# Kernel optimization log

Hardware: AMD Instinct MI355X
Metric: run time of the kernel (lower is better)

The kernel has to match this reference:

```python
import jax, jax.numpy as jnp
import numpy as np
from jax import lax

B, T, D_IN, H, L, D_OUT = 64, 512, 256, 1024, 3, 128


def setup_inputs() -> dict:
    key = jax.random.key(0)
    ks = jax.random.split(key, 8)
    s_in = 1.0 / np.sqrt(H)  # PyTorch-style uniform-ish scale, keeps ReLU recurrence stable
    return {
        "x": jax.random.normal(ks[0], (B, T, D_IN), jnp.float32),
        "w_ih0": jax.random.normal(ks[1], (H, D_IN), jnp.float32) * s_in,
        "w_ih_rest": jax.random.normal(ks[2], (L - 1, H, H), jnp.float32) * s_in,
        "w_hh": jax.random.normal(ks[3], (L, H, H), jnp.float32) * s_in,
        "b_ih": jax.random.normal(ks[4], (L, H), jnp.float32) * s_in,
        "b_hh": jax.random.normal(ks[5], (L, H), jnp.float32) * s_in,
        "fc_w": jax.random.normal(ks[6], (D_OUT, H), jnp.float32) * s_in,
        "fc_b": jax.random.normal(ks[7], (D_OUT,), jnp.float32) * s_in,
    }


def _rnn_layer(seq, w_ih, w_hh, bi, bh):
    # seq: [B, T, d_in]; precompute input projection as one big GEMM
    pre = jnp.einsum("btd,hd->bth", seq, w_ih) + bi + bh  # [B, T, H]
    h0 = jnp.zeros((seq.shape[0], w_hh.shape[0]), seq.dtype)

    def step(h, p_t):  # h: [B, H], p_t: [B, H]
        h = jax.nn.relu(p_t + h @ w_hh.T)
        return h, h

    _, hs = lax.scan(step, h0, jnp.swapaxes(pre, 0, 1))  # [T, B, H]
    return jnp.swapaxes(hs, 0, 1)  # [B, T, H]


def reference(x, w_ih0, w_ih_rest, w_hh, b_ih, b_hh, fc_w, fc_b):
    seq = _rnn_layer(x, w_ih0, w_hh[0], b_ih[0], b_hh[0])
    for l in range(1, L):
        seq = _rnn_layer(seq, w_ih_rest[l - 1], w_hh[l], b_ih[l], b_hh[l])
    # fc on last timestep: out[:, -1, :] @ fc_w.T + fc_b
    return seq[:, -1, :] @ fc_w.T + fc_b
```

## Files before the change

kernel.cpp:

```cpp
#include <hip/hip_runtime.h>

#define NB   64
#define NT   512
#define DIN  256
#define NH   1024
#define DOUT 128

#define HS_STR 1028
#define RD_STR 136

typedef float f4 __attribute__((ext_vector_type(4)));
typedef float f2 __attribute__((ext_vector_type(2)));
typedef unsigned short bfr;

__device__ __forceinline__ float b2f(bfr u) {
    union { unsigned u; float f; } v; v.u = ((unsigned)u) << 16; return v.f;
}
__device__ __forceinline__ bfr f2b(float f) {
    union { float f; unsigned u; } v; v.f = f;
    unsigned r = v.u + 0x7FFFu + ((v.u >> 16) & 1u);
    return (bfr)(r >> 16);
}

template <typename T> __device__ __forceinline__ f4 load4(const T* p);
template <> __device__ __forceinline__ f4 load4<float>(const float* p) { return *(const f4*)p; }
template <> __device__ __forceinline__ f4 load4<bfr>(const bfr* p) {
    ushort4 u = *(const ushort4*)p;
    f4 r; r[0] = b2f(u.x); r[1] = b2f(u.y); r[2] = b2f(u.z); r[3] = b2f(u.w); return r;
}
template <typename T> __device__ __forceinline__ void store1(T* p, float v);
template <> __device__ __forceinline__ void store1<float>(float* p, float v) { *p = v; }
template <> __device__ __forceinline__ void store1<bfr>(bfr* p, float v) { *p = f2b(v); }
template <typename T> __device__ __forceinline__ float load1(const T* p);
template <> __device__ __forceinline__ float load1<float>(const float* p) { return *p; }
template <> __device__ __forceinline__ float load1<bfr>(const bfr* p) { return b2f(*p); }

template <int K, int LOG2CT, typename TA, typename TO>
__global__ __launch_bounds__(256)
void proj_kernel(const TA* __restrict__ A, const float* __restrict__ W,
                 const float* __restrict__ bih, const float* __restrict__ bhh,
                 TO* __restrict__ out, int tOff)
{
    __shared__ float As[16][68];
    __shared__ float Ws[16][68];
    const int tid = threadIdx.x;
    const int CTM = (1 << LOG2CT) - 1;
    const int m0 = (blockIdx.x >> 4) << 6;
    const int n0 = (blockIdx.x & 15) << 6;
    const int tm = tid & 15, tn = tid >> 4;
    const int lr = tid >> 2, lc = tid & 3;

    const int rA = m0 + lr;
    const long mrowA = (long)(rA >> LOG2CT) * NT + tOff + (rA & CTM);

    float acc[4][4] = {};
    for (int k0 = 0; k0 < K; k0 += 16) {
        f4 av = load4<TA>(&A[mrowA * K + k0 + lc * 4]);
        f4 wv = *(const f4*)&W[(n0 + lr) * K + k0 + lc * 4];
        __syncthreads();
        #pragma unroll
        for (int j = 0; j < 4; ++j) {
            As[lc * 4 + j][lr] = av[j];
            Ws[lc * 4 + j][lr] = wv[j];
        }
        __syncthreads();
        #pragma unroll
        for (int k = 0; k < 16; ++k) {
            f4 a = *(const f4*)&As[k][tm * 4];
            f4 w = *(const f4*)&Ws[k][tn * 4];
            #pragma unroll
            for (int i = 0; i < 4; ++i)
                #pragma unroll
                for (int j = 0; j < 4; ++j)
                    acc[i][j] += a[i] * w[j];
        }
    }
    #pragma unroll
    for (int j = 0; j < 4; ++j) {
        const int n = n0 + tn * 4 + j;
        const float bias = bih[n] + bhh[n];
        #pragma unroll
        for (int i = 0; i < 4; ++i)
            store1<TO>(&out[(long)(m0 + tm * 4 + i) * NH + n], acc[i][j] + bias);
    }
}

template <typename TP, int L2CT>
__global__ __launch_bounds__(256)
void copyback_kernel(const TP* __restrict__ Q, TP* __restrict__ P, int tOff)
{
    const int r = blockIdx.x, tid = threadIdx.x;
    const int b = r >> L2CT, t = r & ((1 << L2CT) - 1);
    const TP* q = Q + (long)r * NH;
    TP* p = P + ((long)b * NT + tOff + t) * NH;
    #pragma unroll
    for (int j = 0; j < 4; ++j) p[tid + j * 256] = q[tid + j * 256];
}

template <typename TP>
__global__ __launch_bounds__(512)
void recur_kernel(const float* __restrict__ Whh, TP* __restrict__ P,
                  float* __restrict__ Hring, unsigned* __restrict__ sy)
{
    __shared__ float hsA[8 * HS_STR];
    __shared__ float hsB[8 * HS_STR];
    __shared__ float red[32 * RD_STR];

    const int tid  = threadIdx.x;
    const int wg   = blockIdx.x;
    const int nBase = (wg & 63) << 4;
    const int set   = wg >> 6;
    const int rank  = wg & 63;
    const int lane  = tid & 63;
    const int tk = tid >> 4;
    const int tn = (tid >> 1) & 7;
    const int tb = tid & 1;
    const int bl = tid >> 4;
    const int nl = tid & 15;

    float w0[32], w1[32];
    {
        const float* p0 = &Whh[(nBase + tn * 2 + 0) * NH + tk * 32];
        const float* p1 = &Whh[(nBase + tn * 2 + 1) * NH + tk * 32];
        #pragma unroll
        for (int i = 0; i < 8; ++i) {
            *(f4*)&w0[i * 4] = *(const f4*)&p0[i * 4];
            *(f4*)&w1[i * 4] = *(const f4*)&p1[i * 4];
        }
    }
    for (int i = tid; i < 8 * HS_STR; i += 512) { hsA[i] = 0.f; hsB[i] = 0.f; }
    __syncthreads();

    #pragma unroll 1
    for (int ts = 0; ts < NT; ++ts) {
        const unsigned tgt = (unsigned)(ts + 1);

        float preA = 0.f; TP* ppA = nullptr;
        if (tid < 128) {
            ppA = &P[((long)(set * 16 + bl) * NT + ts) * NH + nBase + nl];
            preA = load1<TP>(ppA);
        }
        {
            float acc[4][2] = {};
            #pragma unroll
            for (int kk = 0; kk < 8; ++kk) {
                f4 hv[4];
                #pragma unroll
                for (int i = 0; i < 4; ++i)
                    hv[i] = *(const f4*)&hsA[(tb * 4 + i) * HS_STR + tk * 32 + kk * 4];
                #pragma unroll
                for (int c = 0; c < 4; ++c)
                    #pragma unroll
                    for (int i = 0; i < 4; ++i) {
                        acc[i][0] += hv[i][c] * w0[kk * 4 + c];
                        acc[i][1] += hv[i][c] * w1[kk * 4 + c];
                    }
            }
            #pragma unroll
            for (int i = 0; i < 4; ++i) {
                red[tk * RD_STR + (tb * 4 + i) * 16 + tn * 2 + 0] = acc[i][0];
                red[tk * RD_STR + (tb * 4 + i) * 16 + tn * 2 + 1] = acc[i][1];
            }
        }
        __syncthreads();
        if (tid < 128) {
            float s = 0.f;
            #pragma unroll
            for (int q = 0; q < 32; ++q) s += red[q * RD_STR + tid];
            const float h = fmaxf(s + preA, 0.f);
            store1<TP>(ppA, h);
            __hip_atomic_store(&Hring[((long)(ts & 1) << 16) + ((set * 16 + bl) << 10) + nBase + nl],
                               h, __ATOMIC_RELAXED, __HIP_MEMORY_SCOPE_AGENT);
        }
        __syncthreads();
        if (tid == 0 && ts < NT - 1)
            __hip_atomic_store(&sy[(set * 2 + 0) * 64 + rank], tgt,
                               __ATOMIC_RELAXED, __HIP_MEMORY_SCOPE_AGENT);

        float preB = 0.f; TP* ppB = nullptr;
        if (tid < 128) {
            ppB = &P[((long)(set * 16 + 8 + bl) * NT + ts) * NH + nBase + nl];
            preB = load1<TP>(ppB);
        }
        {
            float acc[4][2] = {};
            #pragma unroll
            for (int kk = 0; kk < 8; ++kk) {
                f4 hv[4];
                #pragma unroll
                for (int i = 0; i < 4; ++i)
                    hv[i] = *(const f4*)&hsB[(tb * 4 + i) * HS_STR + tk * 32 + kk * 4];
                #pragma unroll
                for (int c = 0; c < 4; ++c)
                    #pragma unroll
                    for (int i = 0; i < 4; ++i) {
                        acc[i][0] += hv[i][c] * w0[kk * 4 + c];
                        acc[i][1] += hv[i][c] * w1[kk * 4 + c];
                    }
            }
            __syncthreads();
            #pragma unroll
            for (int i = 0; i < 4; ++i) {
                red[tk * RD_STR + (tb * 4 + i) * 16 + tn * 2 + 0] = acc[i][0];
                red[tk * RD_STR + (tb * 4 + i) * 16 + tn * 2 + 1] = acc[i][1];
            }
        }
        __syncthreads();
        if (tid < 128) {
            float s = 0.f;
            #pragma unroll
            for (int q = 0; q < 32; ++q) s += red[q * RD_STR + tid];
            const float h = fmaxf(s + preB, 0.f);
            store1<TP>(ppB, h);
            __hip_atomic_store(&Hring[((long)(ts & 1) << 16) + ((set * 16 + 8 + bl) << 10) + nBase + nl],
                               h, __ATOMIC_RELAXED, __HIP_MEMORY_SCOPE_AGENT);
        }
        if (ts == NT - 1) break;
        __syncthreads();
        if (tid == 0)
            __hip_atomic_store(&sy[(set * 2 + 1) * 64 + rank], tgt,
                               __ATOMIC_RELAXED, __HIP_MEMORY_SCOPE_AGENT);

        {
            const unsigned* fpA = &sy[(set * 2 + 0) * 64 + lane];
            const unsigned* fpB = &sy[(set * 2 + 1) * 64 + lane];
            for (;;) {
                unsigned a = __hip_atomic_load(fpA, __ATOMIC_RELAXED, __HIP_MEMORY_SCOPE_AGENT);
                unsigned b = __hip_atomic_load(fpB, __ATOMIC_RELAXED, __HIP_MEMORY_SCOPE_AGENT);
                if (__all((int)(a >= tgt && b >= tgt))) break;
                __builtin_amdgcn_s_sleep(1);
            }
        }

        {
            const float* hbA = Hring + ((long)(ts & 1) << 16) + ((long)(set * 16) << 10) + (tid << 1);
            const float* hbB = hbA + (8 << 10);
            f2 sA[8], sB[8];
            #pragma unroll
            for (int r = 0; r < 8; ++r)
                asm volatile("global_load_dwordx2 %0, %1, off sc0 sc1"
                             : "=v"(sA[r]) : "v"(hbA + (r << 10)) : "memory");
            #pragma unroll
            for (int r = 0; r < 8; ++r)
                asm volatile("global_load_dwordx2 %0, %1, off sc0 sc1"
                             : "=v"(sB[r]) : "v"(hbB + (r << 10)) : "memory");
            asm volatile("s_waitcnt vmcnt(0)" ::: "memory");
            #pragma unroll
            for (int r = 0; r < 8; ++r) {
                *(f2*)&hsA[r * HS_STR + (tid << 1)] = sA[r];
                *(f2*)&hsB[r * HS_STR + (tid << 1)] = sB[r];
            }
        }
        __syncthreads();
    }
}

template <typename TP>
__global__ __launch_bounds__(128)
void fc_kernel(const TP* __restrict__ seq, const float* __restrict__ fcw,
               const float* __restrict__ fcb, float* __restrict__ out)
{
    __shared__ float hrow[NH];
    const int b = blockIdx.x, tid = threadIdx.x;
    for (int i = tid * 4; i < NH; i += 128 * 4) {
        f4 v = load4<TP>(&seq[((long)b * NT + (NT - 1)) * NH + i]);
        *(f4*)&hrow[i] = v;
    }
    __syncthreads();
    float s = 0.f;
    const float* wr = &fcw[tid * NH];
    for (int k = 0; k < NH; k += 4) {
        f4 w = *(const f4*)&wr[k];
        s += w[0] * hrow[k] + w[1] * hrow[k + 1] + w[2] * hrow[k + 2] + w[3] * hrow[k + 3];
    }
    out[b * DOUT + tid] = s + fcb[tid];
}

template <typename TP>
static void coop_recur(const float* W, TP* P, float* Hring, unsigned* sy,
                       hipStream_t stream)
{
    hipMemsetAsync(sy, 0, 4096, stream);
    const float* Wp = W; TP* Pp = P; float* H = Hring; unsigned* s = sy;
    void* args[4] = { &Wp, &Pp, &H, &s };
    hipLaunchCooperativeKernel((const void*)recur_kernel<TP>, dim3(256), dim3(512),
                               args, 0, stream);
}

static void run_pathA(const float* x, const float* wih0, const float* wihr,
                      const float* whh, const float* bih, const float* bhh,
                      const float* fcw, const float* fcb, float* out,
                      unsigned* sy, float* Hring, float* P0, float* P1,
                      hipStream_t stream)
{
    const dim3 blk(256);
    proj_kernel<DIN, 9, float, float><<<8192, blk, 0, stream>>>(x, wih0, bih, bhh, P0, 0);
    coop_recur<float>(whh, P0, Hring, sy, stream);
    proj_kernel<NH, 9, float, float><<<8192, blk, 0, stream>>>(P0, wihr,
        bih + NH, bhh + NH, P1, 0);
    coop_recur<float>(whh + NH * NH, P1, Hring, sy, stream);
    proj_kernel<NH, 9, float, float><<<8192, blk, 0, stream>>>(P1, wihr + NH * NH,
        bih + 2 * NH, bhh + 2 * NH, P0, 0);
    coop_recur<float>(whh + 2 * (NH * NH), P0, Hring, sy, stream);
    fc_kernel<float><<<dim3(NB), dim3(128), 0, stream>>>(P0, fcw, fcb, out);
}

template <typename TP>
static void run_pathBC(const float* x, const float* wih0, const float* wihr,
                       const float* whh, const float* bih, const float* bhh,
                       const float* fcw, const float* fcb, float* out,
                       unsigned* sy, float* Hring, TP* P, TP* Q, hipStream_t stream)
{
    const dim3 blk(256);
    proj_kernel<DIN, 9, float, TP><<<8192, blk, 0, stream>>>(x, wih0, bih, bhh, P, 0);
    coop_recur<TP>(whh, P, Hring, sy, stream);
    for (int l = 1; l < 3; ++l) {
        const float* wih = wihr + (long)(l - 1) * NH * NH;
        for (int c = 0; c < NT / 32; ++c) {
            proj_kernel<NH, 5, TP, TP><<<512, blk, 0, stream>>>(P, wih, bih + l * NH,
                                                                bhh + l * NH, Q, c * 32);
            copyback_kernel<TP, 5><<<NB * 32, blk, 0, stream>>>(Q, P, c * 32);
        }
        coop_recur<TP>(whh + (long)l * NH * NH, P, Hring, sy, stream);
    }
    fc_kernel<TP><<<dim3(NB), dim3(128), 0, stream>>>(P, fcw, fcb, out);
}

extern "C" void kernel_launch(void* const* d_in, const int* in_sizes, int n_in,
                              void* d_out, int out_size, void* d_ws, size_t ws_size,
                              hipStream_t stream)
{
    (void)in_sizes; (void)n_in; (void)out_size;
    const float* x    = (const float*)d_in[0];
    const float* wih0 = (const float*)d_in[1];
    const float* wihr = (const float*)d_in[2];
    const float* whh  = (const float*)d_in[3];
    const float* bih  = (const float*)d_in[4];
    const float* bhh  = (const float*)d_in[5];
    const float* fcw  = (const float*)d_in[6];
    const float* fcb  = (const float*)d_in[7];
    float* out = (float*)d_out;

    char* ws = (char*)d_ws;
    unsigned* sy = (unsigned*)ws;
    float* Hring = (float*)(ws + 4096);
    char* base = ws + 4096 + 2ull * NB * NH * 4;

    const size_t pF32 = (size_t)NB * NT * NH * 4;
    const size_t qF32 = (size_t)NB * 32 * NH * 4;
    const size_t head = 4096 + 2ull * NB * NH * 4;
    const size_t needA = head + 2 * pF32;
    const size_t needB = head + pF32 + qF32;

    if (ws_size >= needA) {
        float* P0 = (float*)base;
        float* P1 = (float*)(base + pF32);
        run_pathA(x, wih0, wihr, whh, bih, bhh, fcw, fcb, out,
                  sy, Hring, P0, P1, stream);
    } else if (ws_size >= needB) {
        float* P = (float*)base;
        float* Q = (float*)(base + pF32);
        run_pathBC<float>(x, wih0, wihr, whh, bih, bhh, fcw, fcb, out,
                          sy, Hring, P, Q, stream);
    } else {
        bfr* P = (bfr*)base;
        bfr* Q = (bfr*)(base + pF32 / 2);
        run_pathBC<bfr>(x, wih0, wihr, whh, bih, bhh, fcw, fcb, out,
                        sy, Hring, P, Q, stream);
    }
}
```

Baseline: 12.30 ms.

## Pipeline batch halves in recurrence so each half's exchange overlaps the other's compute

Restructures the persistent recurrence loop so the two batch halves (A and B) are staggered. Each half publishes its own per-wave ready flags and fetches its hidden state separately, so the poll and global load for one half run while the other half's matvec is in flight. The single full barrier plus combined poll per timestep is removed. The hidden-state tile is also re-laid out in LDS with padding every 32 floats to cut bank conflicts, and flags are polled as 64-bit pairs. The cost is more subtle cross-workgroup ordering and a larger LDS footprint.

New measurement: 10.90 ms. 11.4% less time.

```diff
diff --git a/kernel.cpp b/kernel.cpp
--- a/kernel.cpp
+++ b/kernel.cpp
@@ -6,11 +6,10 @@
 #define NH   1024
 #define DOUT 128
 
-#define HS_STR 1028
-#define RD_STR 136
+#define HS2_STR 1156
+#define RD_STR  136
 
 typedef float f4 __attribute__((ext_vector_type(4)));
-typedef float f2 __attribute__((ext_vector_type(2)));
 typedef unsigned short bfr;
 
 __device__ __forceinline__ float b2f(bfr u) {
@@ -97,13 +96,25 @@
     for (int j = 0; j < 4; ++j) p[tid + j * 256] = q[tid + j * 256];
 }
 
+__device__ __forceinline__ void poll64(const unsigned* fl, unsigned tgt, int lane)
+{
+    const unsigned long long* fp = (const unsigned long long*)fl + lane;
+    for (;;) {
+        unsigned long long v = __hip_atomic_load(fp, __ATOMIC_RELAXED,
+                                                 __HIP_MEMORY_SCOPE_AGENT);
+        unsigned lo = (unsigned)v, hi = (unsigned)(v >> 32);
+        if (__all((int)(lo >= tgt && hi >= tgt))) break;
+        __builtin_amdgcn_s_sleep(1);
+    }
+}
+
 template <typename TP>
 __global__ __launch_bounds__(512)
 void recur_kernel(const float* __restrict__ Whh, TP* __restrict__ P,
                   float* __restrict__ Hring, unsigned* __restrict__ sy)
 {
-    __shared__ float hsA[8 * HS_STR];
-    __shared__ float hsB[8 * HS_STR];
+    __shared__ float hsA[8 * HS2_STR];
+    __shared__ float hsB[8 * HS2_STR];
     __shared__ float red[32 * RD_STR];
 
     const int tid  = threadIdx.x;
@@ -112,11 +123,16 @@
     const int set   = wg >> 6;
     const int rank  = wg & 63;
     const int lane  = tid & 63;
-    const int tk = tid >> 4;
-    const int tn = (tid >> 1) & 7;
-    const int tb = tid & 1;
-    const int bl = tid >> 4;
-    const int nl = tid & 15;
+    const int tk = tid >> 4, tn = (tid >> 1) & 7, tb = tid & 1;
+    const int bl = tid >> 4, nl = tid & 15;
+    const int srow = tid >> 6;
+    const int sgOff = srow * NH + lane * 4;
+    const int slOff = srow * HS2_STR + lane * 4 + ((lane >> 3) << 2);
+
+    unsigned* syA = sy + (set * 2 + 0) * 128;
+    unsigned* syB = sy + (set * 2 + 1) * 128;
+    float* HrA = Hring + (long)(set * 16) * NH;
+    float* HrB = HrA + 8 * NH;
 
     float w0[32], w1[32];
     {
@@ -128,129 +144,135 @@
             *(f4*)&w1[i * 4] = *(const f4*)&p1[i * 4];
         }
     }
-    for (int i = tid; i < 8 * HS_STR; i += 512) { hsA[i] = 0.f; hsB[i] = 0.f; }
+    for (int i = tid; i < 8 * HS2_STR; i += 512) { hsA[i] = 0.f; hsB[i] = 0.f; }
     __syncthreads();
 
     #pragma unroll 1
     for (int ts = 0; ts < NT; ++ts) {
-        const unsigned tgt = (unsigned)(ts + 1);
-
-        float preA = 0.f; TP* ppA = nullptr;
+        const int slot = (ts & 1) * (NB * NH);
+        const int pslot = ((ts - 1) & 1) * (NB * NH);
+
+        float preA = 0.f, preB = 0.f; TP *ppA = nullptr, *ppB = nullptr;
         if (tid < 128) {
             ppA = &P[((long)(set * 16 + bl) * NT + ts) * NH + nBase + nl];
+            ppB = &P[((long)(set * 16 + 8 + bl) * NT + ts) * NH + nBase + nl];
             preA = load1<TP>(ppA);
-        }
-        {
-            float acc[4][2] = {};
-            #pragma unroll
-            for (int kk = 0; kk < 8; ++kk) {
-                f4 hv[4];
+            preB = load1<TP>(ppB);
+        }
+
+        float accA[4][2] = {};
+        #pragma unroll
+        for (int kk = 0; kk < 8; ++kk) {
+            const int kko = tk * 36 + kk * 4;
+            f4 hv[4];
+            #pragma unroll
+            for (int i = 0; i < 4; ++i)
+                hv[i] = *(const f4*)&hsA[(tb * 4 + i) * HS2_STR + kko];
+            #pragma unroll
+            for (int c = 0; c < 4; ++c)
                 #pragma unroll
-                for (int i = 0; i < 4; ++i)
-                    hv[i] = *(const f4*)&hsA[(tb * 4 + i) * HS_STR + tk * 32 + kk * 4];
-                #pragma unroll
-                for (int c = 0; c < 4; ++c)
-                    #pragma unroll
-                    for (int i = 0; i < 4; ++i) {
-                        acc[i][0] += hv[i][c] * w0[kk * 4 + c];
-                        acc[i][1] += hv[i][c] * w1[kk * 4 + c];
-                    }
-            }
-            #pragma unroll
-            for (int i = 0; i < 4; ++i) {
-                red[tk * RD_STR + (tb * 4 + i) * 16 + tn * 2 + 0] = acc[i][0];
-                red[tk * RD_STR + (tb * 4 + i) * 16 + tn * 2 + 1] = acc[i][1];
-            }
-        }
-        __syncthreads();
+                for (int i = 0; i < 4; ++i) {
+                    accA[i][0] += hv[i][c] * w0[kk * 4 + c];
+                    accA[i][1] += hv[i][c] * w1[kk * 4 + c];
+                }
+        }
+
+        f4 sB[4];
+        if (ts > 0) {
+            poll64(syB, (unsigned)ts, lane);
+            const float* src = HrB + pslot + sgOff;
+            #pragma unroll
+            for (int q = 0; q < 4; ++q)
+                asm volatile("global_load_dwordx4 %0, %1, off sc0 sc1"
+                             : "=v"(sB[q]) : "v"(src + q * 256) : "memory");
+        }
+
+        #pragma unroll
+        for (int i = 0; i < 4; ++i) {
+            float* rp = &red[tk * RD_STR + (tb * 4 + i) * 16 + tn * 2];
+            rp[0] = accA[i][0]; rp[1] = accA[i][1];
+        }
+        __syncthreads();
+
         if (tid < 128) {
             float s = 0.f;
             #pragma unroll
             for (int q = 0; q < 32; ++q) s += red[q * RD_STR + tid];
             const float h = fmaxf(s + preA, 0.f);
             store1<TP>(ppA, h);
-            __hip_atomic_store(&Hring[((long)(ts & 1) << 16) + ((set * 16 + bl) << 10) + nBase + nl],
-                               h, __ATOMIC_RELAXED, __HIP_MEMORY_SCOPE_AGENT);
-        }
-        __syncthreads();
-        if (tid == 0 && ts < NT - 1)
-            __hip_atomic_store(&sy[(set * 2 + 0) * 64 + rank], tgt,
+            __hip_atomic_store(&HrA[slot + bl * NH + nBase + nl], h,
                                __ATOMIC_RELAXED, __HIP_MEMORY_SCOPE_AGENT);
-
-        float preB = 0.f; TP* ppB = nullptr;
-        if (tid < 128) {
-            ppB = &P[((long)(set * 16 + 8 + bl) * NT + ts) * NH + nBase + nl];
-            preB = load1<TP>(ppB);
-        }
-        {
-            float acc[4][2] = {};
-            #pragma unroll
-            for (int kk = 0; kk < 8; ++kk) {
-                f4 hv[4];
+            if (ts < NT - 1) {
+                asm volatile("s_waitcnt vmcnt(0)" ::: "memory");
+                if (lane == 0)
+                    __hip_atomic_store(&syA[rank * 2 + (tid >> 6)], (unsigned)(ts + 1),
+                                       __ATOMIC_RELAXED, __HIP_MEMORY_SCOPE_AGENT);
+            }
+        }
+
+        if (ts > 0) {
+            asm volatile("s_waitcnt vmcnt(0)" ::: "memory");
+            #pragma unroll
+            for (int q = 0; q < 4; ++q)
+                *(f4*)&hsB[slOff + q * 288] = sB[q];
+        }
+        __syncthreads();
+
+        float accB[4][2] = {};
+        #pragma unroll
+        for (int kk = 0; kk < 8; ++kk) {
+            const int kko = tk * 36 + kk * 4;
+            f4 hv[4];
+            #pragma unroll
+            for (int i = 0; i < 4; ++i)
+                hv[i] = *(const f4*)&hsB[(tb * 4 + i) * HS2_STR + kko];
+            #pragma unroll
+            for (int c = 0; c < 4; ++c)
                 #pragma unroll
-                for (int i = 0; i < 4; ++i)
-                    hv[i] = *(const f4*)&hsB[(tb * 4 + i) * HS_STR + tk * 32 + kk * 4];
-                #pragma unroll
-                for (int c = 0; c < 4; ++c)
-                    #pragma unroll
-                    for (int i = 0; i < 4; ++i) {
-                        acc[i][0] += hv[i][c] * w0[kk * 4 + c];
-                        acc[i][1] += hv[i][c] * w1[kk * 4 + c];
-                    }
-            }
-            __syncthreads();
-            #pragma unroll
-            for (int i = 0; i < 4; ++i) {
-                red[tk * RD_STR + (tb * 4 + i) * 16 + tn * 2 + 0] = acc[i][0];
-                red[tk * RD_STR + (tb * 4 + i) * 16 + tn * 2 + 1] = acc[i][1];
-            }
-        }
-        __syncthreads();
+                for (int i = 0; i < 4; ++i) {
+                    accB[i][0] += hv[i][c] * w0[kk * 4 + c];
+                    accB[i][1] += hv[i][c] * w1[kk * 4 + c];
+                }
+        }
+
+        f4 sA[4];
+        if (ts < NT - 1) {
+            poll64(syA, (unsigned)(ts + 1), lane);
+            const float* src = HrA + slot + sgOff;
+            #pragma unroll
+            for (int q = 0; q < 4; ++q)
+                asm volatile("global_load_dwordx4 %0, %1, off sc0 sc1"
+                             : "=v"(sA[q]) : "v"(src + q * 256) : "memory");
+        }
+
+        #pragma unroll
+        for (int i = 0; i < 4; ++i) {
+            float* rp = &red[tk * RD_STR + (tb * 4 + i) * 16 + tn * 2];
+            rp[0] = accB[i][0]; rp[1] = accB[i][1];
+        }
+        __syncthreads();
+
         if (tid < 128) {
             float s = 0.f;
             #pragma unroll
             for (int q = 0; q < 32; ++q) s += red[q * RD_STR + tid];
             const float h = fmaxf(s + preB, 0.f);
             store1<TP>(ppB, h);
-            __hip_atomic_store(&Hring[((long)(ts & 1) << 16) + ((set * 16 + 8 + bl) << 10) + nBase + nl],
-                               h, __ATOMIC_RELAXED, __HIP_MEMORY_SCOPE_AGENT);
+            __hip_atomic_store(&HrB[slot + bl * NH + nBase + nl], h,
+                               __ATOMIC_RELAXED, __HIP_MEMORY_SCOPE_AGENT);
+            if (ts < NT - 1) {
+                asm volatile("s_waitcnt vmcnt(0)" ::: "memory");
+                if (lane == 0)
+                    __hip_atomic_store(&syB[rank * 2 + (tid >> 6)], (unsigned)(ts + 1),
+                                       __ATOMIC_RELAXED, __HIP_MEMORY_SCOPE_AGENT);
+            }
         }
         if (ts == NT - 1) break;
-        __syncthreads();
-        if (tid == 0)
-            __hip_atomic_store(&sy[(set * 2 + 1) * 64 + rank], tgt,
-                               __ATOMIC_RELAXED, __HIP_MEMORY_SCOPE_AGENT);
-
-        {
-            const unsigned* fpA = &sy[(set * 2 + 0) * 64 + lane];
-            const unsigned* fpB = &sy[(set * 2 + 1) * 64 + lane];
-            for (;;) {
-                unsigned a = __hip_atomic_load(fpA, __ATOMIC_RELAXED, __HIP_MEMORY_SCOPE_AGENT);
-                unsigned b = __hip_atomic_load(fpB, __ATOMIC_RELAXED, __HIP_MEMORY_SCOPE_AGENT);
-                if (__all((int)(a >= tgt && b >= tgt))) break;
-                __builtin_amdgcn_s_sleep(1);
-            }
-        }
-
-        {
-            const float* hbA = Hring + ((long)(ts & 1) << 16) + ((long)(set * 16) << 10) + (tid << 1);
-            const float* hbB = hbA + (8 << 10);
-            f2 sA[8], sB[8];
-            #pragma unroll
-            for (int r = 0; r < 8; ++r)
-                asm volatile("global_load_dwordx2 %0, %1, off sc0 sc1"
-                             : "=v"(sA[r]) : "v"(hbA + (r << 10)) : "memory");
-            #pragma unroll
-            for (int r = 0; r < 8; ++r)
-                asm volatile("global_load_dwordx2 %0, %1, off sc0 sc1"
-                             : "=v"(sB[r]) : "v"(hbB + (r << 10)) : "memory");
-            asm volatile("s_waitcnt vmcnt(0)" ::: "memory");
-            #pragma unroll
-            for (int r = 0; r < 8; ++r) {
-                *(f2*)&hsA[r * HS_STR + (tid << 1)] = sA[r];
-                *(f2*)&hsB[r * HS_STR + (tid << 1)] = sB[r];
-            }
-        }
+
+        asm volatile("s_waitcnt vmcnt(0)" ::: "memory");
+        #pragma unroll
+        for (int q = 0; q < 4; ++q)
+            *(f4*)&hsA[slOff + q * 288] = sA[q];
         __syncthreads();
     }
 }
```
